# Kernel optimization log

Hardware: AMD Instinct MI355X
Metric: run time of the kernel (lower is better)

Reference implementation:

```python
import jax, jax.numpy as jnp
import numpy as np

N_NODES = 100000
N_EDGES = 3200000
N_GRAPHS = 512
NFEAT, NHID, NCLASS = 64, 32, 16


def setup_inputs() -> dict:
    key = jax.random.key(0)
    ks = jax.random.split(key, 16)
    inp = {
        'solute_x': jax.random.normal(ks[0], (N_NODES, NFEAT), jnp.float32),
        'solvent_x': jax.random.normal(ks[1], (N_NODES, NFEAT), jnp.float32),
        'solute_len_matrix': jax.random.uniform(ks[2], (N_GRAPHS, N_NODES), jnp.float32),
        'solvent_len_matrix': jax.random.uniform(ks[3], (N_GRAPHS, N_NODES), jnp.float32),
        'solute_src': jax.random.randint(ks[4], (N_EDGES,), 0, N_NODES, jnp.int32),
        'solute_dst': jax.random.randint(ks[5], (N_EDGES,), 0, N_NODES, jnp.int32),
        'solvent_src': jax.random.randint(ks[6], (N_EDGES,), 0, N_NODES, jnp.int32),
        'solvent_dst': jax.random.randint(ks[7], (N_EDGES,), 0, N_NODES, jnp.int32),
        'W1': jax.random.normal(ks[8], (NFEAT, NHID), jnp.float32) * 0.05,
        'b1': jnp.zeros((NHID,), jnp.float32),
        'W2': jax.random.normal(ks[9], (NHID, NCLASS), jnp.float32) * 0.05,
        'b2': jnp.zeros((NCLASS,), jnp.float32),
        'fc1_w': jax.random.normal(ks[10], (96, 64), jnp.float32) * 0.05,
        'fc1_b': jnp.zeros((64,), jnp.float32),
        'fc2_w': jax.random.normal(ks[11], (64, 16), jnp.float32) * 0.05,
        'fc2_b': jnp.zeros((16,), jnp.float32),
        'fc3_w': jax.random.normal(ks[12], (16, 1), jnp.float32) * 0.05,
        'fc3_b': jnp.zeros((1,), jnp.float32),
    }
    return inp


def _deg_invsqrt(idx, n):
    # DGL GraphConv norm='both': deg.clamp(min=1) ** -0.5
    deg = jax.ops.segment_sum(jnp.ones_like(idx, jnp.float32), idx, num_segments=n)
    return jax.lax.rsqrt(jnp.maximum(deg, 1.0))


def _gconv(x, W, b, src, dst, src_norm, dst_norm):
    # h' = D_in^{-1/2} A (D_out^{-1/2} x W) + b
    h = (x * src_norm[:, None]) @ W
    agg = jax.ops.segment_sum(h[src], dst, num_segments=x.shape[0])
    return agg * dst_norm[:, None] + b


def reference(solute_x, solvent_x, solute_len_matrix, solvent_len_matrix,
              solute_src, solute_dst, solvent_src, solvent_dst,
              W1, b1, W2, b2, fc1_w, fc1_b, fc2_w, fc2_b, fc3_w, fc3_b):
    n = solute_x.shape[0]
    su_sn = _deg_invsqrt(solute_src, n)   # out-degree norm (src side)
    su_dn = _deg_invsqrt(solute_dst, n)   # in-degree norm (dst side)
    sv_sn = _deg_invsqrt(solvent_src, n)
    sv_dn = _deg_invsqrt(solvent_dst, n)

    su1 = jax.nn.relu(_gconv(solute_x, W1, b1, solute_src, solute_dst, su_sn, su_dn))
    su2 = _gconv(su1, W2, b2, solute_src, solute_dst, su_sn, su_dn)
    sv1 = jax.nn.relu(_gconv(solvent_x, W1, b1, solvent_src, solvent_dst, sv_sn, sv_dn))
    sv2 = _gconv(sv1, W2, b2, solvent_src, solvent_dst, sv_sn, sv_dn)

    # index-matrix readout pooling: [B,N] @ [N,h]
    su1_p = solute_len_matrix @ su1
    su2_p = solute_len_matrix @ su2
    sv1_p = solvent_len_matrix @ sv1
    sv2_p = solvent_len_matrix @ sv2

    data = jnp.concatenate([su1_p, su2_p, sv1_p, sv2_p], axis=1)  # [B, 96]
    data = jax.nn.relu(data @ fc1_w + fc1_b)
    data = jax.nn.relu(data @ fc2_w + fc2_b)
    return data @ fc3_w + fc3_b  # [B, 1]
```

## Files before the change

kernel.cpp:

```cpp
#include <hip/hip_runtime.h>
#include <hip/hip_bf16.h>

#define NN 100000
#define NE 3200000
#define NB 512
#define BINW 128
#define NBINS 782
#define EPB 8192
#define NBLK 391
#define PK 6272
#define PNK 16

typedef unsigned short ushort_t;
typedef unsigned int uint_t;
typedef __attribute__((ext_vector_type(8))) short short8v;
typedef __attribute__((ext_vector_type(4))) float f32x4v;

static __device__ __forceinline__ short f2bf(float f) {
    __hip_bfloat16 h = __float2bfloat16(f);
    return *reinterpret_cast<short*>(&h);
}
static __device__ __forceinline__ float bf2f(ushort_t u) {
    return __uint_as_float(((uint_t)u) << 16);
}

__global__ __launch_bounds__(256) void k_p1(const int* __restrict__ srcA,
                                            const int* __restrict__ dstA,
                                            const int* __restrict__ srcB,
                                            const int* __restrict__ dstB,
                                            int* __restrict__ cnt4,
                                            int* __restrict__ binTot) {
    __shared__ int hD[NBINS], hS[NBINS];
    int t = threadIdx.x, b = blockIdx.x;
    int g = (b >= NBLK) ? 1 : 0;
    int bb = b - g * NBLK;
    const int* src = g ? srcB : srcA;
    const int* dst = g ? dstB : dstA;
    int* cntD = cnt4 + (size_t)(2 * g)     * NBLK * NBINS;
    int* cntS = cnt4 + (size_t)(2 * g + 1) * NBLK * NBINS;
    int* btD  = binTot + (2 * g) * NBINS;
    int* btS  = binTot + (2 * g + 1) * NBINS;
    for (int i = t; i < NBINS; i += 256) { hD[i] = 0; hS[i] = 0; }
    __syncthreads();
    int base = bb * EPB;
#pragma unroll
    for (int i = 0; i < EPB / 1024; i++) {
        int idx = base + i * 1024 + t * 4;
        if (idx < NE) {
            int4 d4 = *(const int4*)(dst + idx);
            int4 s4 = *(const int4*)(src + idx);
            atomicAdd(&hD[d4.x >> 7], 1); atomicAdd(&hD[d4.y >> 7], 1);
            atomicAdd(&hD[d4.z >> 7], 1); atomicAdd(&hD[d4.w >> 7], 1);
            atomicAdd(&hS[s4.x >> 7], 1); atomicAdd(&hS[s4.y >> 7], 1);
            atomicAdd(&hS[s4.z >> 7], 1); atomicAdd(&hS[s4.w >> 7], 1);
        }
    }
    __syncthreads();
    for (int i = t; i < NBINS; i += 256) {
        int vD = hD[i]; cntD[(size_t)bb * NBINS + i] = vD; if (vD) atomicAdd(btD + i, vD);
        int vS = hS[i]; cntS[(size_t)bb * NBINS + i] = vS; if (vS) atomicAdd(btS + i, vS);
    }
}

__global__ void k_scanA(const int* __restrict__ binTot, int* __restrict__ binBase,
                        int* __restrict__ off_su, int* __restrict__ off_sv) {
    __shared__ int s[NBINS];
    int u = blockIdx.x;
    const int* bt = binTot + u * NBINS;
    int* bb = binBase + u * (NBINS + 1);
    int t = threadIdx.x;
    for (int i = t; i < NBINS; i += 256) s[i] = bt[i];
    __syncthreads();
    if (t == 0) {
        int acc = 0;
        for (int i = 0; i < NBINS; i++) { int v = s[i]; s[i] = acc; acc += v; }
    }
    __syncthreads();
    for (int i = t; i < NBINS; i += 256) bb[i] = s[i];
    if (t == 0) bb[NBINS] = NE;
    if (t == 0 && u == 0) { off_su[NN] = NE; off_sv[NN] = NE; }
}

__global__ void k_scanB(int* __restrict__ cnt4, const int* __restrict__ binBase) {
    __shared__ int s[NBLK];
    int u = blockIdx.x / NBINS, j = blockIdx.x % NBINS;
    int* cnt = cnt4 + (size_t)u * NBLK * NBINS;
    const int* bb = binBase + u * (NBINS + 1);
    int t = threadIdx.x;
    for (int i = t; i < NBLK; i += 256) s[i] = cnt[(size_t)i * NBINS + j];
    __syncthreads();
    if (t == 0) {
        int acc = bb[j];
        for (int i = 0; i < NBLK; i++) { int v = s[i]; s[i] = acc; acc += v; }
    }
    __syncthreads();
    for (int i = t; i < NBLK; i += 256) cnt[(size_t)i * NBINS + j] = s[i];
}

__global__ __launch_bounds__(256) void k_p3(const int* __restrict__ src,
                                            const int* __restrict__ dst,
                                            const int* __restrict__ cntD,
                                            const int* __restrict__ cntS,
                                            int2* __restrict__ sortedD,
                                            int* __restrict__ sortedS) {
    __shared__ int curD[NBINS], curS[NBINS];
    int t = threadIdx.x, b = blockIdx.x;
    for (int i = t; i < NBINS; i += 256) {
        curD[i] = cntD[(size_t)b * NBINS + i];
        curS[i] = cntS[(size_t)b * NBINS + i];
    }
    __syncthreads();
    int base = b * EPB;
#pragma unroll
    for (int i = 0; i < EPB / 1024; i++) {
        int idx = base + i * 1024 + t * 4;
        if (idx < NE) {
            int4 s4 = *(const int4*)(src + idx);
            int4 d4 = *(const int4*)(dst + idx);
            int p;
            p = atomicAdd(&curD[d4.x >> 7], 1); sortedD[p] = make_int2(s4.x, d4.x);
            p = atomicAdd(&curD[d4.y >> 7], 1); sortedD[p] = make_int2(s4.y, d4.y);
            p = atomicAdd(&curD[d4.z >> 7], 1); sortedD[p] = make_int2(s4.z, d4.z);
            p = atomicAdd(&curD[d4.w >> 7], 1); sortedD[p] = make_int2(s4.w, d4.w);
            p = atomicAdd(&curS[s4.x >> 7], 1); sortedS[p] = s4.x;
            p = atomicAdd(&curS[s4.y >> 7], 1); sortedS[p] = s4.y;
            p = atomicAdd(&curS[s4.z >> 7], 1); sortedS[p] = s4.z;
            p = atomicAdd(&curS[s4.w >> 7], 1); sortedS[p] = s4.w;
        }
    }
}

__global__ __launch_bounds__(256) void k_p4(const int2* __restrict__ sortedD,
                                            const int* __restrict__ sortedS,
                                            const int* __restrict__ bbD,
                                            const int* __restrict__ bbS,
                                            int* __restrict__ off,
                                            int* __restrict__ edges,
                                            int* __restrict__ cnt_src) {
    __shared__ int hist[BINW], pre[BINW], cur[BINW];
    int t = threadIdx.x;
    if (blockIdx.x < NBINS) {
        int bin = blockIdx.x;
        if (t < BINW) hist[t] = 0;
        __syncthreads();
        int e0 = bbD[bin], e1 = bbD[bin + 1];
        for (int e = e0 + t; e < e1; e += 256)
            atomicAdd(&hist[sortedD[e].y & (BINW - 1)], 1);
        __syncthreads();
        if (t == 0) {
            int a = 0;
            for (int i = 0; i < BINW; i++) { pre[i] = a; a += hist[i]; }
        }
        __syncthreads();
        if (t < BINW) {
            cur[t] = pre[t];
            int node = bin * BINW + t;
            if (node < NN) off[node] = e0 + pre[t];
        }
        __syncthreads();
        for (int e = e0 + t; e < e1; e += 256) {
            int2 ed = sortedD[e];
            int p = atomicAdd(&cur[ed.y & (BINW - 1)], 1);
            edges[e0 + p] = ed.x;
        }
    } else {
        int bin = blockIdx.x - NBINS;
        if (t < BINW) hist[t] = 0;
        __syncthreads();
        int e0 = bbS[bin], e1 = bbS[bin + 1];
        for (int e = e0 + t; e < e1; e += 256)
            atomicAdd(&hist[sortedS[e] & (BINW - 1)], 1);
        __syncthreads();
        if (t < BINW) {
            int node = bin * BINW + t;
            if (node < NN) cnt_src[node] = hist[t];
        }
    }
}

__global__ __launch_bounds__(256) void k_t1(const float* __restrict__ x,
                                            const float* __restrict__ W1,
                                            const int* __restrict__ cnt_src,
                                            ushort_t* __restrict__ y) {
    __shared__ float sW[2048];
    __shared__ float sx[8 * 65];
    int t = threadIdx.x;
    int node0 = blockIdx.x * 8;
    for (int i = t; i < 2048; i += 256) sW[i] = W1[i];
    for (int i = t; i < 512; i += 256) {
        int r = i >> 6, k = i & 63;
        sx[r * 65 + k] = x[(size_t)(node0 + r) * 64 + k];
    }
    __syncthreads();
    int r = t >> 5, c = t & 31;
    int node = node0 + r;
    float sn = rsqrtf(fmaxf((float)cnt_src[node], 1.0f));
    float acc = 0.0f;
#pragma unroll
    for (int k = 0; k < 64; k++) acc += sx[r * 65 + k] * sW[k * 32 + c];
    acc *= sn;
    y[(size_t)node * 32 + c] = (ushort_t)f2bf(acc);
}

__global__ __launch_bounds__(256) void k_t2(const ushort_t* __restrict__ HTb,
                                            const float* __restrict__ W2,
                                            const int* __restrict__ cnt_src,
                                            ushort_t* __restrict__ y2) {
    __shared__ float sW[512];
    __shared__ float sx[16 * 33];
    int t = threadIdx.x;
    int node0 = blockIdx.x * 16;
    for (int i = t; i < 512; i += 256) sW[i] = W2[i];
    for (int i = t; i < 512; i += 256) {
        int r = i & 15, k = i >> 4;
        sx[r * 33 + k] = bf2f(HTb[(size_t)k * NN + node0 + r]);
    }
    __syncthreads();
    int r = t >> 4, c = t & 15;
    int node = node0 + r;
    float sn = rsqrtf(fmaxf((float)cnt_src[node], 1.0f));
    float acc = 0.0f;
#pragma unroll
    for (int k = 0; k < 32; k++) acc += sx[r * 33 + k] * sW[k * 16 + c];
    acc *= sn;
    y2[(size_t)node * 16 + c] = (ushort_t)f2bf(acc);
}

template <int F, int RELU>
__global__ __launch_bounds__(256) void k_agg(
        const uint_t* __restrict__ y, const int* __restrict__ off,
        const int* __restrict__ edges, const float* __restrict__ bias,
        ushort_t* __restrict__ HTb, int coloff) {
    constexpr int L = F / 2;
    constexpr int NPB = 256 / L;
    int t = threadIdx.x;
    int g = t / L, c2 = t % L;
    int node = blockIdx.x * NPB + g;
    int e0 = off[node], e1 = off[node + 1];
    int deg = e1 - e0;
    const int* srow = edges + e0;
    float a0 = 0.0f, a1 = 0.0f;
    int e = 0;
    for (; e + 3 < deg; e += 4) {
        int s0 = srow[e], s1 = srow[e + 1], s2 = srow[e + 2], s3 = srow[e + 3];
        uint_t u0 = y[(size_t)s0 * L + c2];
        uint_t u1 = y[(size_t)s1 * L + c2];
        uint_t u2 = y[(size_t)s2 * L + c2];
        uint_t u3 = y[(size_t)s3 * L + c2];
        a0 += __uint_as_float(u0 << 16) + __uint_as_float(u1 << 16)
            + __uint_as_float(u2 << 16) + __uint_as_float(u3 << 16);
        a1 += __uint_as_float(u0 & 0xFFFF0000u) + __uint_as_float(u1 & 0xFFFF0000u)
            + __uint_as_float(u2 & 0xFFFF0000u) + __uint_as_float(u3 & 0xFFFF0000u);
    }
    for (; e < deg; e++) {
        uint_t u = y[(size_t)srow[e] * L + c2];
        a0 += __uint_as_float(u << 16);
        a1 += __uint_as_float(u & 0xFFFF0000u);
    }
    float dn = rsqrtf(fmaxf((float)deg, 1.0f));
    float v0 = a0 * dn + bias[2 * c2];
    float v1 = a1 * dn + bias[2 * c2 + 1];
    if (RELU) { v0 = fmaxf(v0, 0.0f); v1 = fmaxf(v1, 0.0f); }
    HTb[(size_t)(coloff + 2 * c2) * NN + node] = (ushort_t)f2bf(v0);
    HTb[(size_t)(coloff + 2 * c2 + 1) * NN + node] = (ushort_t)f2bf(v1);
}

__global__ __launch_bounds__(384) void k_pool9(
        const float* __restrict__ lenA, const float* __restrict__ lenB,
        const ushort_t* __restrict__ HTbA, const ushort_t* __restrict__ HTbB,
        float* __restrict__ pooled) {
    __shared__ float red[3][64][4];
    const int mat = blockIdx.z;
    const float* __restrict__ len = mat ? lenB : lenA;
    const ushort_t* __restrict__ HTb = mat ? HTbB : HTbA;
    const int colbase = mat ? 48 : 0;
    const int b0 = blockIdx.x * 16;
    const int w = threadIdx.x >> 6;
    const int l = threadIdx.x & 63;
    const int c = w >> 1;
    const int kh = w & 1;
    const int rc = l & 15;
    const int seg = l >> 4;

    const int kc0 = blockIdx.y * PK;
    const int kend = (kc0 + PK < NN) ? (kc0 + PK) : NN;
    const float* lrow = len + (size_t)(b0 + rc) * NN;
    const ushort_t* hrow = HTb + (size_t)(c * 16 + rc) * NN;

    f32x4v acc = {0.0f, 0.0f, 0.0f, 0.0f};

    const int kw0 = kc0 + kh * 64;
    const int lb0 = kw0 + seg * 8;
    int avail = kend - kw0;
    int Tfull = (avail >= 64) ? ((avail - 64) >> 7) + 1 : 0;

#pragma unroll 2
    for (int t = 0; t < Tfull; t++) {
        int kb = lb0 + t * 128;
#pragma unroll
        for (int h = 0; h < 2; h++) {
            f32x4v a0 = *(const f32x4v*)(lrow + kb + h * 32);
            f32x4v a1 = *(const f32x4v*)(lrow + kb + h * 32 + 4);
            short8v b = *(const short8v*)(hrow + kb + h * 32);
            short8v a;
            a[0] = f2bf(a0.x); a[1] = f2bf(a0.y); a[2] = f2bf(a0.z); a[3] = f2bf(a0.w);
            a[4] = f2bf(a1.x); a[5] = f2bf(a1.y); a[6] = f2bf(a1.z); a[7] = f2bf(a1.w);
            acc = __builtin_amdgcn_mfma_f32_16x16x32_bf16(a, b, acc, 0, 0, 0);
        }
    }

    int kt = kw0 + Tfull * 128;
    if (kt < kend) {
#pragma unroll
        for (int h = 0; h < 2; h++) {
            int kb = kt + h * 32 + seg * 8;
            short8v a = (short8v)0, b = (short8v)0;
            if (kb < kend) {
                f32x4v a0 = *(const f32x4v*)(lrow + kb);
                f32x4v a1 = *(const f32x4v*)(lrow + kb + 4);
                a[0] = f2bf(a0.x); a[1] = f2bf(a0.y); a[2] = f2bf(a0.z); a[3] = f2bf(a0.w);
                a[4] = f2bf(a1.x); a[5] = f2bf(a1.y); a[6] = f2bf(a1.z); a[7] = f2bf(a1.w);
                b = *(const short8v*)(hrow + kb);
            }
            acc = __builtin_amdgcn_mfma_f32_16x16x32_bf16(a, b, acc, 0, 0, 0);
        }
    }

    if (kh == 1) {
        *(f32x4v*)&red[c][l][0] = acc;
    }
    __syncthreads();
    if (kh == 0) {
        f32x4v o = *(const f32x4v*)&red[c][l][0];
#pragma unroll
        for (int r = 0; r < 4; r++) {
            float v = acc[r] + o[r];
            atomicAdd(&pooled[(b0 + seg * 4 + r) * 96 + colbase + c * 16 + rc], v);
        }
    }
}

__global__ void k_mlp(const float* __restrict__ pooled,
                      const float* __restrict__ fc1w, const float* __restrict__ fc1b,
                      const float* __restrict__ fc2w, const float* __restrict__ fc2b,
                      const float* __restrict__ fc3w, const float* __restrict__ fc3b,
                      float* __restrict__ out) {
    __shared__ float srow[96];
    __shared__ float sh[64];
    __shared__ float sh2[16];
    int b = blockIdx.x, t = threadIdx.x;
    srow[t] = pooled[b * 96 + t];
    if (t < 32) srow[64 + t] = pooled[b * 96 + 64 + t];
    __syncthreads();
    float acc = fc1b[t];
    for (int k = 0; k < 96; k++) acc += srow[k] * fc1w[k * 64 + t];
    sh[t] = fmaxf(acc, 0.0f);
    __syncthreads();
    if (t < 16) {
        float a2 = fc2b[t];
        for (int k = 0; k < 64; k++) a2 += sh[k] * fc2w[k * 16 + t];
        sh2[t] = fmaxf(a2, 0.0f);
    }
    __syncthreads();
    if (t == 0) {
        float a3 = fc3b[0];
        for (int k = 0; k < 16; k++) a3 += sh2[k] * fc3w[k];
        out[b] = a3;
    }
}

extern "C" void kernel_launch(void* const* d_in, const int* in_sizes, int n_in,
                              void* d_out, int out_size, void* d_ws, size_t ws_size,
                              hipStream_t stream) {
    const float* solute_x  = (const float*)d_in[0];
    const float* solvent_x = (const float*)d_in[1];
    const float* su_len    = (const float*)d_in[2];
    const float* sv_len    = (const float*)d_in[3];
    const int*   su_src    = (const int*)d_in[4];
    const int*   su_dst    = (const int*)d_in[5];
    const int*   sv_src    = (const int*)d_in[6];
    const int*   sv_dst    = (const int*)d_in[7];
    const float* W1  = (const float*)d_in[8];
    const float* b1  = (const float*)d_in[9];
    const float* W2  = (const float*)d_in[10];
    const float* b2  = (const float*)d_in[11];
    const float* fc1w = (const float*)d_in[12];
    const float* fc1b = (const float*)d_in[13];
    const float* fc2w = (const float*)d_in[14];
    const float* fc2b = (const float*)d_in[15];
    const float* fc3w = (const float*)d_in[16];
    const float* fc3b = (const float*)d_in[17];
    float* out = (float*)d_out;

    char* ws = (char*)d_ws;
    size_t o = 0;
    auto alloc = [&](size_t elems) { void* p = ws + o * 4; o += elems; return p; };
    int* cnt4     = (int*)alloc((size_t)4 * NBLK * NBINS);
    int* binTot   = (int*)alloc(4 * NBINS);
    int* binBase  = (int*)alloc(4 * (NBINS + 1));
    int* off_su   = (int*)alloc(NN + 1);
    int* off_sv   = (int*)alloc(NN + 1);
    int* csrc_su  = (int*)alloc(NN);
    int* csrc_sv  = (int*)alloc(NN);
    float* pooled = (float*)alloc(NB * 96);
    int* edges_su = (int*)alloc(NE);
    int* edges_sv = (int*)alloc(NE);
    o = (o + 1) & ~(size_t)1;
    char* X = ws + o * 4;
    int2*     sortedD = (int2*)X;
    int*      sortedS = (int*)(X + (size_t)NE * 8);
    uint_t*   ybuf    = (uint_t*)X;
    ushort_t* HTb_su  = (ushort_t*)(X + (size_t)NN * 64);
    ushort_t* HTb_sv  = (ushort_t*)(X + (size_t)NN * 160);

    hipMemsetAsync(binTot, 0, 4 * NBINS * 4, stream);
    hipMemsetAsync(pooled, 0, NB * 96 * 4, stream);

    k_p1<<<2 * NBLK, 256, 0, stream>>>(su_src, su_dst, sv_src, sv_dst, cnt4, binTot);
    k_scanA<<<4, 256, 0, stream>>>(binTot, binBase, off_su, off_sv);
    k_scanB<<<4 * NBINS, 256, 0, stream>>>(cnt4, binBase);

    const int* g_src[2]  = {su_src, sv_src};
    const int* g_dst[2]  = {su_dst, sv_dst};
    int* g_off[2]        = {off_su, off_sv};
    int* g_edges[2]      = {edges_su, edges_sv};
    int* g_csrc[2]       = {csrc_su, csrc_sv};

    for (int g = 0; g < 2; g++) {
        const int* cntD = cnt4 + (size_t)(2 * g) * NBLK * NBINS;
        const int* cntS = cnt4 + (size_t)(2 * g + 1) * NBLK * NBINS;
        const int* bbD  = binBase + (2 * g) * (NBINS + 1);
        const int* bbS  = binBase + (2 * g + 1) * (NBINS + 1);
        k_p3<<<NBLK, 256, 0, stream>>>(g_src[g], g_dst[g], cntD, cntS, sortedD, sortedS);
        k_p4<<<2 * NBINS, 256, 0, stream>>>(sortedD, sortedS, bbD, bbS,
                                            g_off[g], g_edges[g], g_csrc[g]);
    }

    const float* g_x[2]  = {solute_x, solvent_x};
    ushort_t* g_HTb[2]   = {HTb_su, HTb_sv};
    for (int g = 0; g < 2; g++) {
        k_t1<<<NN / 8, 256, 0, stream>>>(g_x[g], W1, g_csrc[g], (ushort_t*)ybuf);
        k_agg<32, 1><<<NN / 16, 256, 0, stream>>>(ybuf, g_off[g], g_edges[g], b1, g_HTb[g], 0);
        k_t2<<<NN / 16, 256, 0, stream>>>(g_HTb[g], W2, g_csrc[g], (ushort_t*)ybuf);
        k_agg<16, 0><<<NN / 32, 256, 0, stream>>>(ybuf, g_off[g], g_edges[g], b2, g_HTb[g], 32);
    }

    {
        dim3 gr(NB / 16, PNK, 2);
        k_pool9<<<gr, 384, 0, stream>>>(su_len, sv_len, HTb_su, HTb_sv, pooled);
    }
    k_mlp<<<NB, 64, 0, stream>>>(pooled, fc1w, fc1b, fc2w, fc2b, fc3w, fc3b, out);
}
```

Baseline: 744.9 us.

## Pack sorted edge records and batch both graphs into single kernel launches

Intermediate sort records are packed: each dst-sorted entry becomes a single int holding the src id plus the 7-bit local dst offset, and src-sorted entries shrink to one byte holding the local src offset. This cuts the scatter-write and re-read traffic in the bucketing passes. The solute and solvent graphs are also processed together in each kernel by selecting on block index or blockIdx.y, which halves the launch count and doubles the grid per launch. The exchange is that each graph now needs its own intermediate buffers, and the packing relies on node ids fitting in 20 bits.

```diff
diff --git a/kernel.cpp b/kernel.cpp
--- a/kernel.cpp
+++ b/kernel.cpp
@@ -13,6 +13,7 @@
 
 typedef unsigned short ushort_t;
 typedef unsigned int uint_t;
+typedef unsigned char uchar_t;
 typedef __attribute__((ext_vector_type(8))) short short8v;
 typedef __attribute__((ext_vector_type(4))) float f32x4v;
 
@@ -97,20 +98,30 @@
     for (int i = t; i < NBLK; i += 256) cnt[(size_t)i * NBINS + j] = s[i];
 }
 
-__global__ __launch_bounds__(256) void k_p3(const int* __restrict__ src,
-                                            const int* __restrict__ dst,
-                                            const int* __restrict__ cntD,
-                                            const int* __restrict__ cntS,
-                                            int2* __restrict__ sortedD,
-                                            int* __restrict__ sortedS) {
+__global__ __launch_bounds__(256) void k_p3(const int* __restrict__ srcA,
+                                            const int* __restrict__ dstA,
+                                            const int* __restrict__ srcB,
+                                            const int* __restrict__ dstB,
+                                            const int* __restrict__ cnt4,
+                                            int* __restrict__ sdA, int* __restrict__ sdB,
+                                            uchar_t* __restrict__ ssA,
+                                            uchar_t* __restrict__ ssB) {
     __shared__ int curD[NBINS], curS[NBINS];
     int t = threadIdx.x, b = blockIdx.x;
+    int g = (b >= NBLK) ? 1 : 0;
+    int bb = b - g * NBLK;
+    const int* src = g ? srcB : srcA;
+    const int* dst = g ? dstB : dstA;
+    const int* cntD = cnt4 + (size_t)(2 * g)     * NBLK * NBINS;
+    const int* cntS = cnt4 + (size_t)(2 * g + 1) * NBLK * NBINS;
+    int* sd = g ? sdB : sdA;
+    uchar_t* ss = g ? ssB : ssA;
     for (int i = t; i < NBINS; i += 256) {
-        curD[i] = cntD[(size_t)b * NBINS + i];
-        curS[i] = cntS[(size_t)b * NBINS + i];
-    }
-    __syncthreads();
-    int base = b * EPB;
+        curD[i] = cntD[(size_t)bb * NBINS + i];
+        curS[i] = cntS[(size_t)bb * NBINS + i];
+    }
+    __syncthreads();
+    int base = bb * EPB;
 #pragma unroll
     for (int i = 0; i < EPB / 1024; i++) {
         int idx = base + i * 1024 + t * 4;
@@ -118,34 +129,40 @@
             int4 s4 = *(const int4*)(src + idx);
             int4 d4 = *(const int4*)(dst + idx);
             int p;
-            p = atomicAdd(&curD[d4.x >> 7], 1); sortedD[p] = make_int2(s4.x, d4.x);
-            p = atomicAdd(&curD[d4.y >> 7], 1); sortedD[p] = make_int2(s4.y, d4.y);
-            p = atomicAdd(&curD[d4.z >> 7], 1); sortedD[p] = make_int2(s4.z, d4.z);
-            p = atomicAdd(&curD[d4.w >> 7], 1); sortedD[p] = make_int2(s4.w, d4.w);
-            p = atomicAdd(&curS[s4.x >> 7], 1); sortedS[p] = s4.x;
-            p = atomicAdd(&curS[s4.y >> 7], 1); sortedS[p] = s4.y;
-            p = atomicAdd(&curS[s4.z >> 7], 1); sortedS[p] = s4.z;
-            p = atomicAdd(&curS[s4.w >> 7], 1); sortedS[p] = s4.w;
-        }
-    }
-}
-
-__global__ __launch_bounds__(256) void k_p4(const int2* __restrict__ sortedD,
-                                            const int* __restrict__ sortedS,
-                                            const int* __restrict__ bbD,
-                                            const int* __restrict__ bbS,
-                                            int* __restrict__ off,
-                                            int* __restrict__ edges,
-                                            int* __restrict__ cnt_src) {
+            p = atomicAdd(&curD[d4.x >> 7], 1); sd[p] = s4.x | ((d4.x & 127) << 20);
+            p = atomicAdd(&curD[d4.y >> 7], 1); sd[p] = s4.y | ((d4.y & 127) << 20);
+            p = atomicAdd(&curD[d4.z >> 7], 1); sd[p] = s4.z | ((d4.z & 127) << 20);
+            p = atomicAdd(&curD[d4.w >> 7], 1); sd[p] = s4.w | ((d4.w & 127) << 20);
+            p = atomicAdd(&curS[s4.x >> 7], 1); ss[p] = (uchar_t)(s4.x & 127);
+            p = atomicAdd(&curS[s4.y >> 7], 1); ss[p] = (uchar_t)(s4.y & 127);
+            p = atomicAdd(&curS[s4.z >> 7], 1); ss[p] = (uchar_t)(s4.z & 127);
+            p = atomicAdd(&curS[s4.w >> 7], 1); ss[p] = (uchar_t)(s4.w & 127);
+        }
+    }
+}
+
+__global__ __launch_bounds__(256) void k_p4(const int* __restrict__ sdA,
+                                            const int* __restrict__ sdB,
+                                            const uchar_t* __restrict__ ssA,
+                                            const uchar_t* __restrict__ ssB,
+                                            const int* __restrict__ binBase,
+                                            int* __restrict__ offA, int* __restrict__ offB,
+                                            int* __restrict__ edgesA,
+                                            int* __restrict__ edgesB,
+                                            int* __restrict__ csA, int* __restrict__ csB) {
     __shared__ int hist[BINW], pre[BINW], cur[BINW];
     int t = threadIdx.x;
-    if (blockIdx.x < NBINS) {
-        int bin = blockIdx.x;
+    int u = blockIdx.x / NBINS, bin = blockIdx.x % NBINS;
+    if (u < 2) {
+        const int* sd = u ? sdB : sdA;
+        const int* bb = binBase + (2 * u) * (NBINS + 1);
+        int* off   = u ? offB : offA;
+        int* edges = u ? edgesB : edgesA;
         if (t < BINW) hist[t] = 0;
         __syncthreads();
-        int e0 = bbD[bin], e1 = bbD[bin + 1];
+        int e0 = bb[bin], e1 = bb[bin + 1];
         for (int e = e0 + t; e < e1; e += 256)
-            atomicAdd(&hist[sortedD[e].y & (BINW - 1)], 1);
+            atomicAdd(&hist[sd[e] >> 20], 1);
         __syncthreads();
         if (t == 0) {
             int a = 0;
@@ -159,31 +176,40 @@
         }
         __syncthreads();
         for (int e = e0 + t; e < e1; e += 256) {
-            int2 ed = sortedD[e];
-            int p = atomicAdd(&cur[ed.y & (BINW - 1)], 1);
-            edges[e0 + p] = ed.x;
+            int v = sd[e];
+            int p = atomicAdd(&cur[v >> 20], 1);
+            edges[e0 + p] = v & 0xFFFFF;
         }
     } else {
-        int bin = blockIdx.x - NBINS;
+        const uchar_t* ss = (u == 3) ? ssB : ssA;
+        const int* bb = binBase + (2 * (u - 2) + 1) * (NBINS + 1);
+        int* cs = (u == 3) ? csB : csA;
         if (t < BINW) hist[t] = 0;
         __syncthreads();
-        int e0 = bbS[bin], e1 = bbS[bin + 1];
+        int e0 = bb[bin], e1 = bb[bin + 1];
         for (int e = e0 + t; e < e1; e += 256)
-            atomicAdd(&hist[sortedS[e] & (BINW - 1)], 1);
+            atomicAdd(&hist[ss[e]], 1);
         __syncthreads();
         if (t < BINW) {
             int node = bin * BINW + t;
-            if (node < NN) cnt_src[node] = hist[t];
-        }
-    }
-}
-
-__global__ __launch_bounds__(256) void k_t1(const float* __restrict__ x,
+            if (node < NN) cs[node] = hist[t];
+        }
+    }
+}
+
+__global__ __launch_bounds__(256) void k_t1(const float* __restrict__ xA,
+                                            const float* __restrict__ xB,
                                             const float* __restrict__ W1,
-                                            const int* __restrict__ cnt_src,
-                                            ushort_t* __restrict__ y) {
+                                            const int* __restrict__ csA,
+                                            const int* __restrict__ csB,
+                                            ushort_t* __restrict__ yA,
+                                            ushort_t* __restrict__ yB) {
     __shared__ float sW[2048];
     __shared__ float sx[8 * 65];
+    int g = blockIdx.y;
+    const float* x = g ? xB : xA;
+    const int* cnt_src = g ? csB : csA;
+    ushort_t* y = g ? yB : yA;
     int t = threadIdx.x;
     int node0 = blockIdx.x * 8;
     for (int i = t; i < 2048; i += 256) sW[i] = W1[i];
@@ -202,12 +228,19 @@
     y[(size_t)node * 32 + c] = (ushort_t)f2bf(acc);
 }
 
-__global__ __launch_bounds__(256) void k_t2(const ushort_t* __restrict__ HTb,
+__global__ __launch_bounds__(256) void k_t2(const ushort_t* __restrict__ HTbA,
+                                            const ushort_t* __restrict__ HTbB,
                                             const float* __restrict__ W2,
-                                            const int* __restrict__ cnt_src,
-                                            ushort_t* __restrict__ y2) {
+                                            const int* __restrict__ csA,
+                                            const int* __restrict__ csB,
+                                            ushort_t* __restrict__ yA,
+                                            ushort_t* __restrict__ yB) {
     __shared__ float sW[512];
     __shared__ float sx[16 * 33];
+    int g = blockIdx.y;
+    const ushort_t* HTb = g ? HTbB : HTbA;
+    const int* cnt_src = g ? csB : csA;
+    ushort_t* y2 = g ? yB : yA;
     int t = threadIdx.x;
     int node0 = blockIdx.x * 16;
     for (int i = t; i < 512; i += 256) sW[i] = W2[i];
@@ -228,11 +261,18 @@
 
 template <int F, int RELU>
 __global__ __launch_bounds__(256) void k_agg(
-        const uint_t* __restrict__ y, const int* __restrict__ off,
-        const int* __restrict__ edges, const float* __restrict__ bias,
-        ushort_t* __restrict__ HTb, int coloff) {
+        const uint_t* __restrict__ yA, const uint_t* __restrict__ yB,
+        const int* __restrict__ offA, const int* __restrict__ offB,
+        const int* __restrict__ edgesA, const int* __restrict__ edgesB,
+        const float* __restrict__ bias,
+        ushort_t* __restrict__ HTbA, ushort_t* __restrict__ HTbB, int coloff) {
     constexpr int L = F / 2;
     constexpr int NPB = 256 / L;
+    int gsel = blockIdx.y;
+    const uint_t* y = gsel ? yB : yA;
+    const int* off = gsel ? offB : offA;
+    const int* edges = gsel ? edgesB : edgesA;
+    ushort_t* HTb = gsel ? HTbB : HTbA;
     int t = threadIdx.x;
     int g = t / L, c2 = t % L;
     int node = blockIdx.x * NPB + g;
@@ -407,11 +447,14 @@
     int* edges_sv = (int*)alloc(NE);
     o = (o + 1) & ~(size_t)1;
     char* X = ws + o * 4;
-    int2*     sortedD = (int2*)X;
-    int*      sortedS = (int*)(X + (size_t)NE * 8);
-    uint_t*   ybuf    = (uint_t*)X;
-    ushort_t* HTb_su  = (ushort_t*)(X + (size_t)NN * 64);
-    ushort_t* HTb_sv  = (ushort_t*)(X + (size_t)NN * 160);
+    int*      sdA     = (int*)X;
+    int*      sdB     = (int*)(X + (size_t)NE * 4);
+    uchar_t*  ssA     = (uchar_t*)(X + (size_t)NE * 8);
+    uchar_t*  ssB     = (uchar_t*)(X + (size_t)NE * 9);
+    uint_t*   ybuf_su = (uint_t*)X;
+    uint_t*   ybuf_sv = (uint_t*)(X + (size_t)NN * 64);
+    ushort_t* HTb_su  = (ushort_t*)(X + (size_t)NN * 128);
+    ushort_t* HTb_sv  = (ushort_t*)(X + (size_t)NN * 128 + (size_t)NN * 96);
 
     hipMemsetAsync(binTot, 0, 4 * NBINS * 4, stream);
     hipMemsetAsync(pooled, 0, NB * 96 * 4, stream);
@@ -419,30 +462,24 @@
     k_p1<<<2 * NBLK, 256, 0, stream>>>(su_src, su_dst, sv_src, sv_dst, cnt4, binTot);
     k_scanA<<<4, 256, 0, stream>>>(binTot, binBase, off_su, off_sv);
     k_scanB<<<4 * NBINS, 256, 0, stream>>>(cnt4, binBase);
-
-    const int* g_src[2]  = {su_src, sv_src};
-    const int* g_dst[2]  = {su_dst, sv_dst};
-    int* g_off[2]        = {off_su, off_sv};
-    int* g_edges[2]      = {edges_su, edges_sv};
-    int* g_csrc[2]       = {csrc_su, csrc_sv};
-
-    for (int g = 0; g < 2; g++) {
-        const int* cntD = cnt4 + (size_t)(2 * g) * NBLK * NBINS;
-        const int* cntS = cnt4 + (size_t)(2 * g + 1) * NBLK * NBINS;
-        const int* bbD  = binBase + (2 * g) * (NBINS + 1);
-        const int* bbS  = binBase + (2 * g + 1) * (NBINS + 1);
-        k_p3<<<NBLK, 256, 0, stream>>>(g_src[g], g_dst[g], cntD, cntS, sortedD, sortedS);
-        k_p4<<<2 * NBINS, 256, 0, stream>>>(sortedD, sortedS, bbD, bbS,
-                                            g_off[g], g_edges[g], g_csrc[g]);
-    }
-
-    const float* g_x[2]  = {solute_x, solvent_x};
-    ushort_t* g_HTb[2]   = {HTb_su, HTb_sv};
-    for (int g = 0; g < 2; g++) {
-        k_t1<<<NN / 8, 256, 0, stream>>>(g_x[g], W1, g_csrc[g], (ushort_t*)ybuf);
-        k_agg<32, 1><<<NN / 16, 256, 0, stream>>>(ybuf, g_off[g], g_edges[g], b1, g_HTb[g], 0);
-        k_t2<<<NN / 16, 256, 0, stream>>>(g_HTb[g], W2, g_csrc[g], (ushort_t*)ybuf);
-        k_agg<16, 0><<<NN / 32, 256, 0, stream>>>(ybuf, g_off[g], g_edges[g], b2, g_HTb[g], 32);
+    k_p3<<<2 * NBLK, 256, 0, stream>>>(su_src, su_dst, sv_src, sv_dst, cnt4,
+                                       sdA, sdB, ssA, ssB);
+    k_p4<<<4 * NBINS, 256, 0, stream>>>(sdA, sdB, ssA, ssB, binBase,
+                                        off_su, off_sv, edges_su, edges_sv,
+                                        csrc_su, csrc_sv);
+
+    {
+        dim3 g1(NN / 8, 2);
+        k_t1<<<g1, 256, 0, stream>>>(solute_x, solvent_x, W1, csrc_su, csrc_sv,
+                                     (ushort_t*)ybuf_su, (ushort_t*)ybuf_sv);
+        dim3 g2(NN / 16, 2);
+        k_agg<32, 1><<<g2, 256, 0, stream>>>(ybuf_su, ybuf_sv, off_su, off_sv,
+                                             edges_su, edges_sv, b1, HTb_su, HTb_sv, 0);
+        k_t2<<<g2, 256, 0, stream>>>(HTb_su, HTb_sv, W2, csrc_su, csrc_sv,
+                                     (ushort_t*)ybuf_su, (ushort_t*)ybuf_sv);
+        dim3 g3(NN / 32, 2);
+        k_agg<16, 0><<<g3, 256, 0, stream>>>(ybuf_su, ybuf_sv, off_su, off_sv,
+                                             edges_su, edges_sv, b2, HTb_su, HTb_sv, 32);
     }
 
     {
```

New measurement: 706.6 us. 5.1% less time.
